# Optimization experiments

Measured on AMD Instinct MI355X. Metric: run time of the kernel, lower is better.

## Reference

```python
import jax, jax.numpy as jnp
import numpy as np

B, S, E = 4, 1024, 1280
H = 16
D = E // H  # 80


def rotate_half(x):
    x1, x2 = jnp.split(x, 2, axis=-1)
    return jnp.concatenate([-x2, x1], axis=-1)


def setup_inputs() -> dict:
    key = jax.random.key(0)
    ks = jax.random.split(key, 12)
    sc = 0.02
    x = jax.random.normal(ks[0], (B, S, E), dtype=jnp.float32)
    # variable per-item sequence lengths (each <= S), cumulative
    lens = np.array([1024, 896, 768, 640], dtype=np.int32)
    cu_seqlens = jnp.asarray(np.concatenate([[0], np.cumsum(lens)]), dtype=jnp.int32)
    # rotary cos/sin for positions 0..S-1, head_dim D
    inv_freq = 1.0 / (10000.0 ** (np.arange(0, D, 2, dtype=np.float32) / D))
    t = np.arange(S, dtype=np.float32)
    freqs = np.outer(t, inv_freq)               # [S, D/2]
    emb = np.concatenate([freqs, freqs], axis=-1)  # [S, D]
    cos = jnp.asarray(np.cos(emb), dtype=jnp.float32)
    sin = jnp.asarray(np.sin(emb), dtype=jnp.float32)
    wq = jax.random.normal(ks[1], (E, E), dtype=jnp.float32) * sc
    bq = jax.random.normal(ks[2], (E,), dtype=jnp.float32) * sc
    wk = jax.random.normal(ks[3], (E, E), dtype=jnp.float32) * sc
    bk = jax.random.normal(ks[4], (E,), dtype=jnp.float32) * sc
    wv = jax.random.normal(ks[5], (E, E), dtype=jnp.float32) * sc
    bv = jax.random.normal(ks[6], (E,), dtype=jnp.float32) * sc
    wo = jax.random.normal(ks[7], (E, E), dtype=jnp.float32) * sc
    bo = jax.random.normal(ks[8], (E,), dtype=jnp.float32) * sc
    return {"x": x, "cu_seqlens": cu_seqlens, "cos": cos, "sin": sin,
            "wq": wq, "bq": bq, "wk": wk, "bk": bk, "wv": wv, "bv": bv,
            "wo": wo, "bo": bo}


def reference(x, cu_seqlens, cos, sin, wq, bq, wk, bk, wv, bv, wo, bo):
    b, s, e = x.shape
    h, d = H, D
    # QKV projections (nn.Linear: x @ W^T + b)
    q = (x @ wq.T + bq).reshape(b, s, h, d)
    k = (x @ wk.T + bk).reshape(b, s, h, d)
    v = (x @ wv.T + bv).reshape(b, s, h, d)
    # rotary embedding (apply_rotary_pos_emb, 'normal')
    c = cos[None, :, None, :]  # [1, s, 1, d]
    sn = sin[None, :, None, :]
    q = q * c + rotate_half(q) * sn
    k = k * c + rotate_half(k) * sn
    # patch attention mask from cu_seqlens (flatten_batch=False):
    # token i attends to token j iff i < len_b and j < len_b
    seq_lens = cu_seqlens[1:] - cu_seqlens[:-1]          # [b]
    idx = jnp.arange(s)
    valid = idx[None, :] < seq_lens[:, None]             # [b, s]
    mask = valid[:, None, :, None] & valid[:, None, None, :]  # [b, 1, s, s]
    # SDPA, non-causal
    scale = 1.0 / jnp.sqrt(jnp.asarray(d, dtype=q.dtype))
    scores = jnp.einsum("bqhd,bkhd->bhqk", q, k) * scale
    scores = jnp.where(mask, scores, jnp.asarray(-1e9, dtype=scores.dtype))
    attn = jax.nn.softmax(scores, axis=-1)
    out = jnp.einsum("bhqk,bkhd->bqhd", attn, v)         # [b, s, h, d]
    out = out.reshape(b, s, e)
    # output projection
    return out @ wo.T + bo
```

## Files before the change

kernel.cpp:

```cpp
#include <hip/hip_runtime.h>
#include <hip/hip_bf16.h>

#define B_ 4
#define S_ 1024
#define E_ 1280
#define H_ 16
#define D_ 80
#define M_ (B_*S_)
#define QBLK 128

typedef __hip_bfloat16 bf16;
using bf16x8 = __attribute__((ext_vector_type(8))) short;
using f32x4  = __attribute__((ext_vector_type(4))) float;

__device__ __forceinline__ float b2f(bf16 x){ return __bfloat162float(x); }
__device__ __forceinline__ bf16  f2b(float x){ return __float2bfloat16(x); }
__device__ __forceinline__ void  stf(float* p, float v){ *p = v; }
__device__ __forceinline__ void  stf(bf16*  p, float v){ *p = f2b(v); }

__device__ __forceinline__ void gload_lds16(const void* g, void* l) {
    __builtin_amdgcn_global_load_lds(
        (const __attribute__((address_space(1))) unsigned int*)g,
        (__attribute__((address_space(3))) unsigned int*)l, 16, 0, 0);
}

__global__ __launch_bounds__(256) void cvt_kernel(
    const float* __restrict__ s0, const float* __restrict__ s1,
    const float* __restrict__ s2, const float* __restrict__ s3,
    const float* __restrict__ s4,
    bf16* __restrict__ d0, bf16* __restrict__ d1, bf16* __restrict__ d2,
    bf16* __restrict__ d3, bf16* __restrict__ d4,
    int n0, int n1)
{
    const float* s; bf16* d; int n;
    switch (blockIdx.y) {
        case 0: s = s0; d = d0; n = n0; break;
        case 1: s = s1; d = d1; n = n1; break;
        case 2: s = s2; d = d2; n = n1; break;
        case 3: s = s3; d = d3; n = n1; break;
        default: s = s4; d = d4; n = n1; break;
    }
    int i = (blockIdx.x * 256 + threadIdx.x) * 8;
    if (i >= n) return;
    float4 a = *(const float4*)(s + i);
    float4 b = *(const float4*)(s + i + 4);
    bf16 t[8];
    t[0]=f2b(a.x); t[1]=f2b(a.y); t[2]=f2b(a.z); t[3]=f2b(a.w);
    t[4]=f2b(b.x); t[5]=f2b(b.y); t[6]=f2b(b.z); t[7]=f2b(b.w);
    *(uint4*)(d + i) = *(const uint4*)t;
}

template<typename TC, bool VT_OUT>
__global__ __launch_bounds__(256) void mfma_gemm_bt(
    const bf16* __restrict__ A,
    const bf16* __restrict__ W0, const bf16* __restrict__ W1, const bf16* __restrict__ W2,
    const float* __restrict__ b0, const float* __restrict__ b1, const float* __restrict__ b2,
    TC* __restrict__ C0, TC* __restrict__ C1, TC* __restrict__ C2,
    int K, int N, int ntiles)
{
    const int mat = blockIdx.y / ntiles;
    const int bn  = (blockIdx.y % ntiles) * 128;
    const int bm  = blockIdx.x * 128;
    const bf16* W; const float* bias; TC* C;
    if (mat == 0)      { W = W0; bias = b0; C = C0; }
    else if (mat == 1) { W = W1; bias = b1; C = C1; }
    else               { W = W2; bias = b2; C = C2; }

    __shared__ bf16 As[2][128][32];
    __shared__ bf16 Ws[2][128][32];

    const int tid  = threadIdx.x;
    const int lane = tid & 63;
    const int wv   = tid >> 6;
    const int wm   = (wv & 1) * 64;
    const int wn   = (wv >> 1) * 64;
    const int srow = wv * 16 + (lane >> 2);
    const int scol = (lane & 3) * 8;

    f32x4 acc[4][4] = {};

    for (int k0 = 0; k0 < K; k0 += 64) {
        __syncthreads();
        #pragma unroll
        for (int p = 0; p < 2; p++) {
            const int kc = k0 + p*32 + scol;
            gload_lds16(A + (size_t)(bm + srow)      * K + kc, &As[p][wv*16][0]);
            gload_lds16(A + (size_t)(bm + 64 + srow) * K + kc, &As[p][64 + wv*16][0]);
            gload_lds16(W + (size_t)(bn + srow)      * K + kc, &Ws[p][wv*16][0]);
            gload_lds16(W + (size_t)(bn + 64 + srow) * K + kc, &Ws[p][64 + wv*16][0]);
        }
        __syncthreads();

        const int fr = lane & 15;
        const int kq = (lane >> 4) * 8;
        #pragma unroll
        for (int p = 0; p < 2; p++) {
            bf16x8 af[4], wf[4];
            #pragma unroll
            for (int t = 0; t < 4; t++) {
                af[t] = *(const bf16x8*)&As[p][wm + t*16 + fr][kq];
                wf[t] = *(const bf16x8*)&Ws[p][wn + t*16 + fr][kq];
            }
            #pragma unroll
            for (int mt = 0; mt < 4; mt++)
                #pragma unroll
                for (int nt = 0; nt < 4; nt++)
                    acc[mt][nt] = __builtin_amdgcn_mfma_f32_16x16x32_bf16(
                        af[mt], wf[nt], acc[mt][nt], 0, 0, 0);
        }
    }

    const int col_l = lane & 15;
    const int row_l = (lane >> 4) * 4;

    if (VT_OUT && mat == 2) {
        const int btok = bm >> 10;
        const int keyb = (bm & 1023) + wm + row_l;
        #pragma unroll
        for (int nt = 0; nt < 4; nt++) {
            const int n = bn + wn + nt*16 + col_l;
            const float bv = bias[n];
            const int hh = n / 80, dd = n % 80;
            bf16* vbase = (bf16*)C + ((size_t)(btok*H_ + hh)*D_ + dd)*S_ + keyb;
            #pragma unroll
            for (int mt = 0; mt < 4; mt++) {
                union { bf16 h[4]; uint2 u; } t4;
                #pragma unroll
                for (int r = 0; r < 4; r++) t4.h[r] = f2b(acc[mt][nt][r] + bv);
                *(uint2*)&vbase[mt*16] = t4.u;
            }
        }
    } else {
        #pragma unroll
        for (int nt = 0; nt < 4; nt++) {
            const int n = bn + wn + nt*16 + col_l;
            const float bv = bias[n];
            #pragma unroll
            for (int mt = 0; mt < 4; mt++) {
                #pragma unroll
                for (int r = 0; r < 4; r++) {
                    const int m = bm + wm + mt*16 + row_l + r;
                    stf(&C[(size_t)m * N + n], acc[mt][nt][r] + bv);
                }
            }
        }
    }
}

__device__ __forceinline__ void rope8(const bf16* lo, const bf16* hi,
                                      const float* cp, const float* sp,
                                      float mul, uint4* out_lo, uint4* out_hi)
{
    union { uint4 u; bf16 h[8]; } li, hi_, lo_o, hi_o;
    li.u  = *(const uint4*)lo;
    hi_.u = *(const uint4*)hi;
    #pragma unroll
    for (int u = 0; u < 8; u++) {
        float x1 = b2f(li.h[u]), x2 = b2f(hi_.h[u]);
        float c = cp[u], s = sp[u];
        lo_o.h[u] = f2b((x1*c - x2*s) * mul);
        hi_o.h[u] = f2b((x2*c + x1*s) * mul);
    }
    *out_lo = lo_o.u;
    *out_hi = hi_o.u;
}

__global__ __launch_bounds__(256) void rope_kernel(
    bf16* __restrict__ qp, bf16* __restrict__ kp,
    const float* __restrict__ cosp, const float* __restrict__ sinp)
{
    int idx = blockIdx.x * 256 + threadIdx.x;
    const int NT = M_ * H_ * 5;
    bf16* base; float mul;
    if (idx < NT) { base = qp; mul = 0.11180339887498949f; }
    else         { base = kp; mul = 1.0f; idx -= NT; }
    const int row = idx / 80;
    const int rem = idx - row * 80;
    const int h   = rem / 5;
    const int pc  = rem - h * 5;
    const int s   = row & (S_ - 1);
    bf16* p = base + (size_t)row * E_ + h * D_ + pc * 8;
    const float* cp = cosp + s * D_ + pc * 8;
    const float* sp = sinp + s * D_ + pc * 8;
    uint4 olo, ohi;
    rope8(p, p + 40, cp, sp, mul, &olo, &ohi);
    *(uint4*)p        = olo;
    *(uint4*)(p + 40) = ohi;
}

__global__ __launch_bounds__(512, 4) void attn_mfma(
    const bf16* __restrict__ q, const bf16* __restrict__ k, const bf16* __restrict__ vt,
    const int* __restrict__ cu, bf16* __restrict__ o)
{
    __shared__ __align__(16) bf16 Ks[2][64*80];
    __shared__ __align__(16) bf16 VTs[2][80*64];
    __shared__ __align__(16) bf16 PTs[8][16*76];

    const int n  = blockIdx.x;
    const int g  = ((n >> 6) << 3) | (n & 7);
    const int qs = (n >> 3) & 7;
    const int b  = g >> 4;
    const int h  = g & 15;

    const int tid  = threadIdx.x;
    const int lane = tid & 63, wv = tid >> 6;
    const int quad = lane >> 4, l15 = lane & 15;
    const int q0   = qs * QBLK;
    const int len  = cu[b + 1] - cu[b];

    const bool uniformq = (q0 >= len);
    const bool clean    = ((len & (QBLK - 1)) == 0);
    const int  ktiles   = uniformq ? 16 : (clean ? (len >> 6) : 16);
    const bool domask   = !uniformq && !clean;

    bf16* PT = &PTs[wv][0];

    bf16x8 qf[3] = {};
    if (!uniformq) {
        const bf16* qrow = q + (size_t)(b*S_ + q0 + wv*16 + l15)*E_ + h*D_ + quad*8;
        qf[0] = *(const bf16x8*)(qrow);
        qf[1] = *(const bf16x8*)(qrow + 32);
        if (quad < 2) qf[2] = *(const bf16x8*)(qrow + 64);
    } else {
        const bf16 one = f2b(1.0f);
        #pragma unroll
        for (int nt = 0; nt < 4; nt++)
            #pragma unroll
            for (int r = 0; r < 4; r++)
                PT[(quad*4 + r)*76 + nt*16 + l15] = one;
    }

    float m_r[4], l_r[4];
    #pragma unroll
    for (int r = 0; r < 4; r++) { m_r[r] = -1e30f; l_r[r] = 0.f; }
    f32x4 o_acc[5] = {};

    const int u_  = l15 >> 2;
    const int s0r = quad ^ u_;
    const int sv0 = quad ^ (l15 & 7);

    auto stage = [&](int kt, int bf) {
        #pragma unroll
        for (int i = 0; i < 3; i++) {
            int c = tid + i * 512;
            if (c < 640) {
                if (!uniformq) {
                    int row = c / 10, s5 = c - row * 10;
                    int uu = (row >> 2) & 3;
                    int sg = (s5 < 8) ? (s5 ^ uu) : (8 + ((s5 ^ uu) & 1));
                    gload_lds16(k + (size_t)(b*S_ + kt*64 + row)*E_ + h*D_ + sg*8,
                                &Ks[bf][c*8]);
                }
            } else if (c < 1280) {
                int c2 = c - 640;
                int row = c2 >> 3, s5 = c2 & 7;
                int sg = s5 ^ (row & 7);
                gload_lds16(vt + ((size_t)(b*H_ + h)*D_ + row)*S_ + kt*64 + sg*8,
                            &VTs[bf][c2*8]);
            }
        }
    };

    stage(0, 0);
    __syncthreads();

    const bool q_full = (q0 + 64) <= len;

    for (int kt = 0; kt < ktiles; kt++) {
        const int cur = kt & 1;
        if (kt + 1 < ktiles) stage(kt + 1, cur ^ 1);

        if (!uniformq) {
            f32x4 s4[4];
            #pragma unroll
            for (int nt = 0; nt < 4; nt++) {
                const bf16* kr = &Ks[cur][(nt*16 + l15) * 80];
                bf16x8 kf0 = *(const bf16x8*)(kr + s0r*8);
                bf16x8 kf1 = *(const bf16x8*)(kr + 32 + s0r*8);
                bf16x8 kf2 = {};
                if (quad < 2) kf2 = *(const bf16x8*)(kr + 64 + (s0r & 1)*8);
                f32x4 a0 = {};
                a0 = __builtin_amdgcn_mfma_f32_16x16x32_bf16(qf[0], kf0, a0, 0, 0, 0);
                a0 = __builtin_amdgcn_mfma_f32_16x16x32_bf16(qf[1], kf1, a0, 0, 0, 0);
                a0 = __builtin_amdgcn_mfma_f32_16x16x32_bf16(qf[2], kf2, a0, 0, 0, 0);
                s4[nt] = a0;
            }

            float sv[4][4];
            if (!domask || (q_full && (kt*64 + 64) <= len)) {
                #pragma unroll
                for (int r = 0; r < 4; r++)
                    #pragma unroll
                    for (int nt = 0; nt < 4; nt++)
                        sv[nt][r] = s4[nt][r];
            } else {
                bool vk[4];
                #pragma unroll
                for (int nt = 0; nt < 4; nt++) vk[nt] = (kt*64 + nt*16 + l15) < len;
                #pragma unroll
                for (int r = 0; r < 4; r++) {
                    const bool vq = (q0 + wv*16 + quad*4 + r) < len;
                    #pragma unroll
                    for (int nt = 0; nt < 4; nt++)
                        sv[nt][r] = (vq && vk[nt]) ? s4[nt][r] : -1e9f;
                }
            }
            float rmax[4];
            #pragma unroll
            for (int r = 0; r < 4; r++)
                rmax[r] = fmaxf(fmaxf(sv[0][r], sv[1][r]), fmaxf(sv[2][r], sv[3][r]));
            #pragma unroll
            for (int st = 1; st < 16; st <<= 1)
                #pragma unroll
                for (int r = 0; r < 4; r++)
                    rmax[r] = fmaxf(rmax[r], __shfl_xor(rmax[r], st, 64));
            float mnew[4], alpha[4], rsum[4], p[4][4];
            #pragma unroll
            for (int r = 0; r < 4; r++) {
                mnew[r]  = fmaxf(m_r[r], rmax[r]);
                alpha[r] = __expf(m_r[r] - mnew[r]);
                float a = 0.f;
                #pragma unroll
                for (int nt = 0; nt < 4; nt++) { p[nt][r] = __expf(sv[nt][r] - mnew[r]); a += p[nt][r]; }
                rsum[r] = a;
            }
            #pragma unroll
            for (int st = 1; st < 16; st <<= 1)
                #pragma unroll
                for (int r = 0; r < 4; r++)
                    rsum[r] += __shfl_xor(rsum[r], st, 64);
            #pragma unroll
            for (int r = 0; r < 4; r++) {
                l_r[r] = l_r[r] * alpha[r] + rsum[r];
                m_r[r] = mnew[r];
            }
            #pragma unroll
            for (int dt = 0; dt < 5; dt++)
                #pragma unroll
                for (int r = 0; r < 4; r++)
                    o_acc[dt][r] *= alpha[r];
            #pragma unroll
            for (int nt = 0; nt < 4; nt++)
                #pragma unroll
                for (int r = 0; r < 4; r++)
                    PT[(quad*4 + r)*76 + nt*16 + l15] = f2b(p[nt][r]);
        }

        bf16x8 pa0 = *(const bf16x8*)&PT[l15*76 + quad*8];
        bf16x8 pa1 = *(const bf16x8*)&PT[l15*76 + 32 + quad*8];
        #pragma unroll
        for (int dt = 0; dt < 5; dt++) {
            const bf16* vr = &VTs[cur][(dt*16 + l15) * 64];
            bf16x8 vf0 = *(const bf16x8*)(vr + sv0*8);
            bf16x8 vf1 = *(const bf16x8*)(vr + (sv0 ^ 4)*8);
            o_acc[dt] = __builtin_amdgcn_mfma_f32_16x16x32_bf16(pa0, vf0, o_acc[dt], 0, 0, 0);
            o_acc[dt] = __builtin_amdgcn_mfma_f32_16x16x32_bf16(pa1, vf1, o_acc[dt], 0, 0, 0);
        }
        __syncthreads();
    }

    #pragma unroll
    for (int r = 0; r < 4; r++) {
        const float inv = uniformq ? (1.0f / 1024.0f) : (1.0f / l_r[r]);
        size_t row_g = (size_t)(b*S_ + q0 + wv*16 + quad*4 + r);
        #pragma unroll
        for (int dt = 0; dt < 5; dt++)
            o[row_g*E_ + h*D_ + dt*16 + l15] = f2b(o_acc[dt][r] * inv);
    }
}

extern "C" void kernel_launch(void* const* d_in, const int* in_sizes, int n_in,
                              void* d_out, int out_size, void* d_ws, size_t ws_size,
                              hipStream_t stream)
{
    const float* x    = (const float*)d_in[0];
    const int*   cu   = (const int*)  d_in[1];
    const float* cosp = (const float*)d_in[2];
    const float* sinp = (const float*)d_in[3];
    const float* wq   = (const float*)d_in[4];
    const float* bq   = (const float*)d_in[5];
    const float* wk   = (const float*)d_in[6];
    const float* bk   = (const float*)d_in[7];
    const float* wv   = (const float*)d_in[8];
    const float* bv   = (const float*)d_in[9];
    const float* wo   = (const float*)d_in[10];
    const float* bo   = (const float*)d_in[11];
    float* out = (float*)d_out;

    bf16* q   = (bf16*)d_ws;
    bf16* kk  = q   + (size_t)M_ * E_;
    bf16* vt  = kk  + (size_t)M_ * E_;
    bf16* ao  = vt  + (size_t)M_ * E_;
    bf16* xb  = ao  + (size_t)M_ * E_;
    bf16* wqb = xb  + (size_t)M_ * E_;
    bf16* wkb = wqb + (size_t)E_ * E_;
    bf16* wvb = wkb + (size_t)E_ * E_;
    bf16* wob = wvb + (size_t)E_ * E_;

    cvt_kernel<<<dim3(2560, 5), 256, 0, stream>>>(
        x, wq, wk, wv, wo, xb, wqb, wkb, wvb, wob, M_*E_, E_*E_);

    mfma_gemm_bt<bf16, true><<<dim3(M_/128, 30), 256, 0, stream>>>(
        xb, wqb, wkb, wvb, bq, bk, bv, q, kk, vt, E_, E_, 10);

    rope_kernel<<<2560, 256, 0, stream>>>(q, kk, cosp, sinp);

    attn_mfma<<<512, 512, 0, stream>>>(q, kk, vt, cu, ao);

    mfma_gemm_bt<float, false><<<dim3(M_/128, 10), 256, 0, stream>>>(
        ao, wob, wob, wob, bo, bo, bo, out, out, out, E_, E_, 10);
}
```

Baseline: 269.2 us.

## Replace QKV GEMM with 256x256-tile, 8-phase pipelined MFMA kernel

Adds a new QKV projection kernel that uses 256x256 output tiles with 512 threads and double-buffered LDS filled by direct global-to-LDS loads. Each iteration is split into eight phases that interleave async prefetch of the next K-slices with MFMA groups, using barriers, s_setprio and partial vmcnt waits. The larger tiles are meant to raise arithmetic intensity and cut global traffic, and the phased schedule is meant to hide load latency behind compute. The cost is higher register and LDS pressure and a grid of only 240 blocks, which may leave compute units poorly balanced.

After: 254.5 us. 1.06x faster.

```diff
diff --git a/kernel.cpp b/kernel.cpp
--- a/kernel.cpp
+++ b/kernel.cpp
@@ -22,6 +22,30 @@
     __builtin_amdgcn_global_load_lds(
         (const __attribute__((address_space(1))) unsigned int*)g,
         (__attribute__((address_space(3))) unsigned int*)l, 16, 0, 0);
+}
+
+__device__ __forceinline__ void ph_begin() {
+    __builtin_amdgcn_s_barrier();
+    asm volatile("s_waitcnt lgkmcnt(0)" ::: "memory");
+    __builtin_amdgcn_sched_barrier(0);
+    __builtin_amdgcn_s_setprio(1);
+}
+__device__ __forceinline__ void ph_end() {
+    __builtin_amdgcn_s_setprio(0);
+    __builtin_amdgcn_sched_barrier(0);
+    __builtin_amdgcn_s_barrier();
+}
+__device__ __forceinline__ void ph_end_vm6() {
+    __builtin_amdgcn_s_setprio(0);
+    __builtin_amdgcn_sched_barrier(0);
+    asm volatile("s_waitcnt vmcnt(6)" ::: "memory");
+    __builtin_amdgcn_s_barrier();
+}
+__device__ __forceinline__ void ph_end_vm0() {
+    __builtin_amdgcn_s_setprio(0);
+    __builtin_amdgcn_sched_barrier(0);
+    asm volatile("s_waitcnt vmcnt(0)" ::: "memory");
+    __builtin_amdgcn_s_barrier();
 }
 
 __global__ __launch_bounds__(256) void cvt_kernel(
@@ -48,6 +72,153 @@
     t[0]=f2b(a.x); t[1]=f2b(a.y); t[2]=f2b(a.z); t[3]=f2b(a.w);
     t[4]=f2b(b.x); t[5]=f2b(b.y); t[6]=f2b(b.z); t[7]=f2b(b.w);
     *(uint4*)(d + i) = *(const uint4*)t;
+}
+
+__global__ __launch_bounds__(512, 2) void qkv_gemm_8ph(
+    const bf16* __restrict__ A,
+    const bf16* __restrict__ W0, const bf16* __restrict__ W1, const bf16* __restrict__ W2,
+    const float* __restrict__ b0, const float* __restrict__ b1, const float* __restrict__ b2,
+    bf16* __restrict__ Cq, bf16* __restrict__ Ck, bf16* __restrict__ Cv)
+{
+    constexpr int K = 1280;
+    constexpr int NITER = K / 128;
+
+    __shared__ __align__(16) bf16 Asm[2][2][128*64];
+    __shared__ __align__(16) bf16 Bsm[2][2][128*64];
+
+    const int bm  = blockIdx.x * 256;
+    const int ny  = blockIdx.y;
+    const int mat = ny / 5;
+    const int bn  = (ny % 5) * 256;
+    const bf16*  W    = (mat == 0) ? W0 : (mat == 1) ? W1 : W2;
+    const float* bias = (mat == 0) ? b0 : (mat == 1) ? b1 : b2;
+
+    const int tid  = threadIdx.x;
+    const int lane = tid & 63, wv = tid >> 6;
+    const int wm = wv >> 2, wn = wv & 3;
+    const int quad = lane >> 4, l15 = lane & 15;
+
+    auto stageA = [&](int j_, int half) {
+        #pragma unroll
+        for (int i = 0; i < 2; i++) {
+            const int c   = tid + i*512;
+            const int row = c >> 3;
+            const int g   = (c & 7) ^ (row & 7);
+            gload_lds16(A + (size_t)(bm + half*128 + row) * K + j_*64 + g*8,
+                        &Asm[j_ & 1][half][(wv*64 + i*512) * 8]);
+        }
+    };
+    auto stageB = [&](int j_, int half) {
+        #pragma unroll
+        for (int i = 0; i < 2; i++) {
+            const int c   = tid + i*512;
+            const int row = c >> 3;
+            const int g   = (c & 7) ^ (row & 7);
+            gload_lds16(W + (size_t)(bn + half*128 + row) * K + j_*64 + g*8,
+                        &Bsm[j_ & 1][half][(wv*64 + i*512) * 8]);
+        }
+    };
+    auto lda = [&](int bf, int mt, int ks) -> bf16x8 {
+        const int r = mt*16 + l15;
+        return *(const bf16x8*)&Asm[bf][wm][r*64 + (((quad + ks*4) ^ (r & 7)) << 3)];
+    };
+    auto ldb = [&](int bf, int nt, int ks) -> bf16x8 {
+        const int r = (wn & 1)*64 + nt*16 + l15;
+        return *(const bf16x8*)&Bsm[bf][wn >> 1][r*64 + (((quad + ks*4) ^ (r & 7)) << 3)];
+    };
+
+    f32x4 acc[8][4] = {};
+    bf16x8 a[4][2], bA[2][2], bB[2][2];
+
+#define MFMA_Q(MT0, NT0, BB_) do { \
+    _Pragma("unroll") for (int mt_ = 0; mt_ < 4; mt_++) \
+    _Pragma("unroll") for (int nt_ = 0; nt_ < 2; nt_++) \
+    _Pragma("unroll") for (int ks_ = 0; ks_ < 2; ks_++) \
+        acc[(MT0)+mt_][(NT0)+nt_] = __builtin_amdgcn_mfma_f32_16x16x32_bf16( \
+            a[mt_][ks_], BB_[nt_][ks_], acc[(MT0)+mt_][(NT0)+nt_], 0, 0, 0); \
+} while (0)
+
+    stageA(0, 0); stageA(0, 1); stageB(0, 0); stageB(0, 1);
+    stageA(1, 0); stageA(1, 1); stageB(1, 0); stageB(1, 1);
+    __syncthreads();
+
+    for (int t = 0; t < NITER; t++) {
+        const int  j  = 2*t;
+        const bool pf = (t + 1 < NITER);
+
+        #pragma unroll
+        for (int mt = 0; mt < 4; mt++) { a[mt][0] = lda(0, mt, 0); a[mt][1] = lda(0, mt, 1); }
+        #pragma unroll
+        for (int nt = 0; nt < 2; nt++) { bA[nt][0] = ldb(0, nt, 0); bA[nt][1] = ldb(0, nt, 1); }
+        stageA(j+1, 1);
+        ph_begin(); MFMA_Q(0, 0, bA); ph_end();
+
+        #pragma unroll
+        for (int nt = 0; nt < 2; nt++) { bB[nt][0] = ldb(0, 2+nt, 0); bB[nt][1] = ldb(0, 2+nt, 1); }
+        ph_begin(); MFMA_Q(0, 2, bB); ph_end();
+
+        #pragma unroll
+        for (int mt = 0; mt < 4; mt++) { a[mt][0] = lda(0, 4+mt, 0); a[mt][1] = lda(0, 4+mt, 1); }
+        if (pf) stageB(j+2, 0);
+        ph_begin(); MFMA_Q(4, 0, bA); ph_end();
+
+        if (pf) { stageB(j+2, 1); stageA(j+2, 0); }
+        ph_begin(); MFMA_Q(4, 2, bB);
+        if (pf) ph_end_vm6(); else ph_end_vm0();
+
+        #pragma unroll
+        for (int mt = 0; mt < 4; mt++) { a[mt][0] = lda(1, mt, 0); a[mt][1] = lda(1, mt, 1); }
+        #pragma unroll
+        for (int nt = 0; nt < 2; nt++) { bA[nt][0] = ldb(1, nt, 0); bA[nt][1] = ldb(1, nt, 1); }
+        if (pf) stageA(j+2, 1);
+        ph_begin(); MFMA_Q(0, 0, bA); ph_end();
+
+        #pragma unroll
+        for (int nt = 0; nt < 2; nt++) { bB[nt][0] = ldb(1, 2+nt, 0); bB[nt][1] = ldb(1, 2+nt, 1); }
+        ph_begin(); MFMA_Q(0, 2, bB); ph_end();
+
+        #pragma unroll
+        for (int mt = 0; mt < 4; mt++) { a[mt][0] = lda(1, 4+mt, 0); a[mt][1] = lda(1, 4+mt, 1); }
+        if (pf) stageB(j+3, 0);
+        ph_begin(); MFMA_Q(4, 0, bA); ph_end();
+
+        if (pf) { stageB(j+3, 1); stageA(j+3, 0); }
+        ph_begin(); MFMA_Q(4, 2, bB); ph_end_vm6();
+    }
+#undef MFMA_Q
+
+    if (mat < 2) {
+        bf16* C = (mat == 0) ? Cq : Ck;
+        #pragma unroll
+        for (int nt = 0; nt < 4; nt++) {
+            const int ncol = bn + wn*64 + nt*16 + l15;
+            const float bv = bias[ncol];
+            #pragma unroll
+            for (int mt = 0; mt < 8; mt++) {
+                const int m0 = bm + wm*128 + mt*16 + quad*4;
+                #pragma unroll
+                for (int r = 0; r < 4; r++)
+                    C[(size_t)(m0 + r) * E_ + ncol] = f2b(acc[mt][nt][r] + bv);
+            }
+        }
+    } else {
+        #pragma unroll
+        for (int nt = 0; nt < 4; nt++) {
+            const int ncol = bn + wn*64 + nt*16 + l15;
+            const float bv = bias[ncol];
+            const int hh = ncol / 80, dd = ncol % 80;
+            #pragma unroll
+            for (int mt = 0; mt < 8; mt++) {
+                const int m0  = bm + wm*128 + mt*16 + quad*4;
+                const int btok = m0 >> 10;
+                const int key  = m0 & 1023;
+                union { bf16 h[4]; uint2 u; } t4;
+                #pragma unroll
+                for (int r = 0; r < 4; r++) t4.h[r] = f2b(acc[mt][nt][r] + bv);
+                *(uint2*)&Cv[((size_t)(btok*H_ + hh)*D_ + dd)*S_ + key] = t4.u;
+            }
+        }
+    }
 }
 
 template<typename TC, bool VT_OUT>
@@ -400,8 +571,8 @@
     cvt_kernel<<<dim3(2560, 5), 256, 0, stream>>>(
         x, wq, wk, wv, wo, xb, wqb, wkb, wvb, wob, M_*E_, E_*E_);
 
-    mfma_gemm_bt<bf16, true><<<dim3(M_/128, 30), 256, 0, stream>>>(
-        xb, wqb, wkb, wvb, bq, bk, bv, q, kk, vt, E_, E_, 10);
+    qkv_gemm_8ph<<<dim3(M_/256, 15), 512, 0, stream>>>(
+        xb, wqb, wkb, wvb, bq, bk, bv, q, kk, vt);
 
     rope_kernel<<<2560, 256, 0, stream>>>(q, kk, cosp, sinp);
 
```
